# Optimization experiments

Hardware: AMD Instinct MI355X
Metric: run time of the kernel (lower is better)

Reference implementation:

```python
import jax, jax.numpy as jnp
import numpy as np

ALPHA = 0.15       # blend weight for merged mean vs center token
SIZE_DELTA = 0.0   # additive smoothing on cluster sizes


def setup_inputs() -> dict:
    key = jax.random.key(0)
    B, T, C = 8, 4096, 1024
    x = jax.random.normal(key, (B, T, C), dtype=jnp.float32)
    return {"x": x, "layer_idx": 0, "requested_r": 2048}


def reference(x, layer_idx, requested_r):
    B, T, C = x.shape
    K = max(1, T - int(requested_r))

    # token importance scores = squared L2 norm per token
    scores = jnp.sum(x * x, axis=-1)                      # [B, T]
    # CLS protection: force token 0 to be kept
    scores = scores.at[:, 0].set(jnp.finfo(scores.dtype).max)
    _, keep_idx = jax.lax.top_k(scores, K)                # [B, K]
    keep_idx = jnp.sort(keep_idx, axis=-1)

    # cosine nearest-kept-center assignment
    feat = x / (jnp.linalg.norm(x, axis=-1, keepdims=True) + 1e-12)  # [B, T, C]
    kept_feat = jnp.take_along_axis(feat, keep_idx[..., None], axis=1)  # [B, K, C]
    sim = jnp.einsum('bth,bkh->btk', feat, kept_feat)     # [B, T, K]
    assign_idx = jnp.argmax(sim, axis=-1)                 # [B, T]
    # force each kept center to self-assign (vectorized scatter,
    # replaces the original Python double for-loop with .item() syncs)
    b_idx = jnp.arange(B)[:, None]
    assign_idx = assign_idx.at[b_idx, keep_idx].set(jnp.arange(K)[None, :])

    # scatter-based size-weighted merge: segment mean over assigned tokens
    seg = (assign_idx + jnp.arange(B)[:, None] * K).reshape(-1)       # [B*T]
    sums = jax.ops.segment_sum(x.reshape(B * T, C), seg, num_segments=B * K)
    cnt = jax.ops.segment_sum(jnp.ones((B * T,), x.dtype), seg, num_segments=B * K)
    merged = (sums / (cnt[:, None] + SIZE_DELTA)).reshape(B, K, C)    # [B, K, C]

    x_kept = jnp.take_along_axis(x, keep_idx[..., None], axis=1)      # [B, K, C]
    out = (1.0 - ALPHA) * x_kept + ALPHA * merged
    return out
```

## Files before the change

kernel.cpp:

```cpp
#include <hip/hip_runtime.h>
#include <hip/hip_bf16.h>
#include <float.h>
#include <math.h>

constexpr int B_ = 8;
constexpr int T_ = 4096;
constexpr int C_ = 1024;
constexpr int K_ = 2048;
constexpr int MROWS = T_ - K_;

constexpr int BM = 128, BN = 128, BK = 64;
constexpr int NB = K_ / BN;
constexpr float REFINE_DELTA = 4e-4f;

typedef _Float16 f16x8 __attribute__((ext_vector_type(8)));
typedef float    f32x4 __attribute__((ext_vector_type(4)));

__device__ __forceinline__ void gload16(const ushort* g, ushort* l) {
  __builtin_amdgcn_global_load_lds(
      (const __attribute__((address_space(1))) unsigned int*)g,
      (__attribute__((address_space(3))) unsigned int*)l, 16, 0, 0);
}

__global__ __launch_bounds__(256) void split_score_kernel(
    const float* __restrict__ x, ushort* __restrict__ xh,
    double* __restrict__ sd, float* __restrict__ rnorm)
{
  int lane = threadIdx.x & 63, wave = threadIdx.x >> 6;
  int row = blockIdx.x * 4 + wave;
  size_t base = (size_t)row * C_;
  double s = 0.0;
  #pragma unroll
  for (int j = 0; j < 4; j++) {
    int i4 = j * 256 + lane * 4;
    float4 v = *reinterpret_cast<const float4*>(&x[base + i4]);
    ushort4 h;
    { _Float16 a = (_Float16)v.x; h.x = *(ushort*)&a; }
    { _Float16 a = (_Float16)v.y; h.y = *(ushort*)&a; }
    { _Float16 a = (_Float16)v.z; h.z = *(ushort*)&a; }
    { _Float16 a = (_Float16)v.w; h.w = *(ushort*)&a; }
    *reinterpret_cast<ushort4*>(&xh[base + i4]) = h;
    s += (double)v.x * v.x + (double)v.y * v.y
       + (double)v.z * v.z + (double)v.w * v.w;
  }
  #pragma unroll
  for (int off = 32; off > 0; off >>= 1) s += __shfl_down(s, off);
  if (lane == 0) {
    sd[row] = s;
    rnorm[row] = (float)(1.0 / (sqrt(s) + 1e-12));
  }
}

__global__ __launch_bounds__(256) void rank_kernel(
    const double* __restrict__ sd, int* __restrict__ flag)
{
  int b = blockIdx.y;
  __shared__ double sh[T_];
  for (int i = threadIdx.x; i < T_; i += 256)
    sh[i] = (i == 0) ? DBL_MAX : sd[b * T_ + i];
  __syncthreads();
  int t = blockIdx.x * 128 + (threadIdx.x >> 1);
  int half = threadIdx.x & 1;
  double key = sh[t];
  int cnt = 0;
  int j0 = half * 2048;
  #pragma unroll 4
  for (int jj = 0; jj < 2048; jj++) {
    int j = j0 + jj;
    double sj = sh[j];
    cnt += (sj > key) || (sj == key && j < t);
  }
  cnt += __shfl_xor(cnt, 1);
  if (half == 0) flag[b * T_ + t] = (cnt < K_) ? 1 : 0;
}

__global__ __launch_bounds__(256) void select_kernel(
    const int* __restrict__ flag, int* __restrict__ keep_idx,
    int* __restrict__ drop_idx, int* __restrict__ assign)
{
  int b = blockIdx.x, tid = threadIdx.x;
  __shared__ int sums[256];
  int f[16], s = 0;
  int base = b * T_ + tid * 16;
  #pragma unroll
  for (int i = 0; i < 16; i++) { f[i] = flag[base + i]; s += f[i]; }
  sums[tid] = s;
  __syncthreads();
  for (int off = 1; off < 256; off <<= 1) {
    int v = 0;
    if (tid >= off) v = sums[tid - off];
    __syncthreads();
    if (tid >= off) sums[tid] += v;
    __syncthreads();
  }
  int run = (tid == 0) ? 0 : sums[tid - 1];
  #pragma unroll
  for (int i = 0; i < 16; i++) {
    int t = tid * 16 + i;
    if (f[i]) { keep_idx[b * K_ + run] = t; assign[b * T_ + t] = run; run++; }
    else drop_idx[b * MROWS + (t - run)] = t;
  }
}

__global__ void zero_kernel(int* __restrict__ cnt, int* __restrict__ nref)
{
  int i = blockIdx.x * 256 + threadIdx.x;
  if (i < B_ * K_) cnt[i] = 0;
  if (i == 0) *nref = 0;
}

__global__ __launch_bounds__(256) void mfma_argmax_kernel(
    const ushort* __restrict__ xh, const float* __restrict__ rnorm,
    const int* __restrict__ keep_idx, const int* __restrict__ drop_idx,
    float* __restrict__ pb, float* __restrict__ ps, int* __restrict__ pk)
{
  __shared__ __align__(16) ushort lds[2][2][8][128][8];

  int b  = blockIdx.z;
  int m0 = blockIdx.y * BM;
  int n0 = blockIdx.x * BN;
  int tid = threadIdx.x;
  int lane = tid & 63, wave = tid >> 6;
  int quad = lane >> 4, col = lane & 15;
  int wm = wave >> 1, wn = wave & 1;

  int srow = tid & 127;
  int sc8  = (tid >> 7) * 8;

  int dtok_s = drop_idx[b * MROWS + m0 + srow];
  const ushort* ga = xh + (size_t)(b * T_ + dtok_s) * C_;
  int ktok_s = keep_idx[b * K_ + n0 + srow];
  const ushort* gb = xh + (size_t)(b * T_ + ktok_s) * C_;

  int ldst = tid * 8;

  float scale[4]; int ncand[4];
  #pragma unroll
  for (int j = 0; j < 4; j++) {
    int nn = n0 + wn * 64 + j * 16 + col;
    ncand[j] = nn;
    scale[j] = rnorm[b * T_ + keep_idx[b * K_ + nn]];
  }

  f32x4 acc[4][4];
  #pragma unroll
  for (int i = 0; i < 4; i++)
    #pragma unroll
    for (int j = 0; j < 4; j++) acc[i][j] = (f32x4)0.f;

  auto issue = [&](int k0, int st) {
    ushort* base = &lds[st][0][0][0][0];
    gload16(ga + k0 + sc8,      base + ldst);
    gload16(ga + k0 + 16 + sc8, base + ldst + 2048);
    gload16(ga + k0 + 32 + sc8, base + ldst + 4096);
    gload16(ga + k0 + 48 + sc8, base + ldst + 6144);
    ushort* bb = base + 8192;
    gload16(gb + k0 + sc8,      bb + ldst);
    gload16(gb + k0 + 16 + sc8, bb + ldst + 2048);
    gload16(gb + k0 + 32 + sc8, bb + ldst + 4096);
    gload16(gb + k0 + 48 + sc8, bb + ldst + 6144);
  };

  issue(0, 0);
  __syncthreads();

  for (int ks = 0; ks < C_ / BK; ks++) {
    int cur = ks & 1;
    if (ks < C_ / BK - 1) issue((ks + 1) * BK, cur ^ 1);

    #pragma unroll
    for (int s = 0; s < 2; s++) {
      f16x8 fa[4], fb[4];
      #pragma unroll
      for (int i = 0; i < 4; i++) {
        int row = wm * 64 + i * 16 + col;
        fa[i] = *reinterpret_cast<const f16x8*>(&lds[cur][0][s * 4 + quad][row][0]);
      }
      #pragma unroll
      for (int j = 0; j < 4; j++) {
        int row = wn * 64 + j * 16 + col;
        fb[j] = *reinterpret_cast<const f16x8*>(&lds[cur][1][s * 4 + quad][row][0]);
      }
      #pragma unroll
      for (int i = 0; i < 4; i++)
        #pragma unroll
        for (int j = 0; j < 4; j++)
          acc[i][j] = __builtin_amdgcn_mfma_f32_16x16x32_f16(fa[i], fb[j], acc[i][j], 0, 0, 0);
    }
    __syncthreads();
  }

  float* redb   = (float*)(&lds[0][0][0][0][0]);
  float* redsec = redb + 256;
  int*   redk   = (int*)(redb + 512);

  #pragma unroll
  for (int i = 0; i < 4; i++) {
    #pragma unroll
    for (int r = 0; r < 4; r++) {
      float b1 = -FLT_MAX, b2 = -FLT_MAX; int k1 = 0;
      #pragma unroll
      for (int j = 0; j < 4; j++) {
        float v = acc[i][j][r] * scale[j];
        if (v > b1) { b2 = b1; b1 = v; k1 = ncand[j]; }
        else if (v > b2) b2 = v;
      }
      #pragma unroll
      for (int off = 1; off < 16; off <<= 1) {
        float ob1 = __shfl_xor(b1, off);
        float ob2 = __shfl_xor(b2, off);
        int   ok1 = __shfl_xor(k1, off);
        if (ob1 > b1 || (ob1 == b1 && ok1 < k1)) { b2 = fmaxf(b1, ob2); b1 = ob1; k1 = ok1; }
        else b2 = fmaxf(b2, ob1);
      }
      if (col == 0) {
        int tl = wm * 64 + i * 16 + quad * 4 + r;
        redb[wn * 128 + tl] = b1; redsec[wn * 128 + tl] = b2; redk[wn * 128 + tl] = k1;
      }
    }
  }
  __syncthreads();
  if (tid < 128) {
    float b1 = redb[tid], b2 = redsec[tid]; int k1 = redk[tid];
    float o1 = redb[128 + tid], o2 = redsec[128 + tid]; int ok = redk[128 + tid];
    if (o1 > b1) { b2 = fmaxf(b1, o2); b1 = o1; k1 = ok; }
    else b2 = fmaxf(b2, o1);
    size_t p = ((size_t)(b * NB + blockIdx.x)) * MROWS + m0 + tid;
    pb[p] = b1; ps[p] = b2; pk[p] = k1;
  }
}

__global__ __launch_bounds__(256) void reduce2_kernel(
    const float* __restrict__ pb, const float* __restrict__ ps, const int* __restrict__ pk,
    const float* __restrict__ rnorm, const int* __restrict__ drop_idx,
    int* __restrict__ assign, int* __restrict__ rlist, int* __restrict__ nref)
{
  int idx2 = blockIdx.x * 256 + threadIdx.x;
  int b = idx2 >> 11;
  int rc = idx2 & (MROWS - 1);
  float b1 = -FLT_MAX, b2 = -FLT_MAX; int k1 = 0;
  for (int nb = 0; nb < NB; nb++) {
    size_t p = ((size_t)(b * NB + nb)) * MROWS + rc;
    float v = pb[p], s = ps[p]; int k = pk[p];
    if (v > b1) { b2 = fmaxf(b1, s); b1 = v; k1 = k; }
    else b2 = fmaxf(b2, v);
  }
  int t = drop_idx[idx2];
  assign[b * T_ + t] = k1;
  if ((b1 - b2) * rnorm[b * T_ + t] < REFINE_DELTA) {
    int qi = atomicAdd(nref, 1);
    rlist[qi] = idx2;
  }
}

__global__ __launch_bounds__(256) void refine_kernel(
    const float* __restrict__ x, const double* __restrict__ sd,
    const int* __restrict__ keep_idx, const int* __restrict__ drop_idx,
    const float* __restrict__ rnorm,
    const float* __restrict__ pb, const float* __restrict__ ps, const int* __restrict__ pk,
    const int* __restrict__ nref, const int* __restrict__ rlist, int* __restrict__ assign)
{
  __shared__ __align__(16) float xs[C_];
  __shared__ int cand[K_];
  __shared__ int ncand_s;
  __shared__ double wv[4];
  __shared__ int wk[4];
  __shared__ float spb[NB], sps[NB];
  __shared__ int spk[NB];
  int n = *nref;
  int lane = threadIdx.x & 63, wave = threadIdx.x >> 6;
  for (int qi = blockIdx.x; qi < n; qi += gridDim.x) {
    int idx2 = rlist[qi];
    int b = idx2 >> 11, rc = idx2 & (MROWS - 1);
    int t = drop_idx[idx2];
    int bt = b * T_ + t;
    __syncthreads();
    const float* xt = x + ((size_t)b * T_ + t) * C_;
    for (int i = threadIdx.x; i < C_; i += 256) xs[i] = xt[i];
    if (threadIdx.x < NB) {
      size_t p = ((size_t)(b * NB + threadIdx.x)) * MROWS + rc;
      spb[threadIdx.x] = pb[p]; sps[threadIdx.x] = ps[p]; spk[threadIdx.x] = pk[p];
    }
    __syncthreads();
    if (threadIdx.x == 0) {
      float b1 = -FLT_MAX;
      for (int nb = 0; nb < NB; nb++) if (spb[nb] > b1) b1 = spb[nb];
      float thr = b1 - REFINE_DELTA / rnorm[bt];
      int nc = 0;
      for (int nb = 0; nb < NB; nb++) {
        if (spb[nb] >= thr) {
          if (sps[nb] >= thr) { for (int j = 0; j < BN; j++) cand[nc++] = nb * BN + j; }
          else cand[nc++] = spk[nb];
        }
      }
      ncand_s = nc;
    }
    __syncthreads();
    int nc = ncand_s;
    double bv = -DBL_MAX; int bk = 0x7fffffff;
    for (int ci = wave; ci < nc; ci += 4) {
      int k = cand[ci];
      int kt = keep_idx[b * K_ + k];
      const float* xr = x + ((size_t)b * T_ + kt) * C_;
      double s = 0.0;
      int c0 = lane * 16;
      #pragma unroll
      for (int c = 0; c < 16; c += 4) {
        float4 v = *reinterpret_cast<const float4*>(&xr[c0 + c]);
        s += (double)xs[c0 + c]     * v.x + (double)xs[c0 + c + 1] * v.y
           + (double)xs[c0 + c + 2] * v.z + (double)xs[c0 + c + 3] * v.w;
      }
      #pragma unroll
      for (int off = 32; off > 0; off >>= 1) s += __shfl_down(s, off);
      s = __shfl(s, 0);
      s /= sqrt(sd[b * T_ + kt]);
      if (s > bv || (s == bv && k < bk)) { bv = s; bk = k; }
    }
    if (lane == 0) { wv[wave] = bv; wk[wave] = bk; }
    __syncthreads();
    if (threadIdx.x == 0) {
      double fb = wv[0]; int fk = wk[0];
      for (int w2 = 1; w2 < 4; w2++)
        if (wv[w2] > fb || (wv[w2] == fb && wk[w2] < fk)) { fb = wv[w2]; fk = wk[w2]; }
      assign[bt] = fk;
    }
  }
}

__global__ void count_kernel(const int* __restrict__ assign, int* __restrict__ cnt)
{
  int i = blockIdx.x * 256 + threadIdx.x;
  int b = i >> 12;
  atomicAdd(&cnt[b * K_ + assign[i]], 1);
}

__global__ __launch_bounds__(256) void scan_kernel(
    const int* __restrict__ cnt, int* __restrict__ offs, int* __restrict__ cursor)
{
  int b = blockIdx.x, tid = threadIdx.x;
  __shared__ int sums[256];
  int v[8], s = 0;
  int base = b * K_ + tid * 8;
  #pragma unroll
  for (int i = 0; i < 8; i++) { v[i] = cnt[base + i]; s += v[i]; }
  sums[tid] = s;
  __syncthreads();
  for (int off = 1; off < 256; off <<= 1) {
    int t2 = 0;
    if (tid >= off) t2 = sums[tid - off];
    __syncthreads();
    if (tid >= off) sums[tid] += t2;
    __syncthreads();
  }
  int run = (tid == 0) ? 0 : sums[tid - 1];
  #pragma unroll
  for (int i = 0; i < 8; i++) { offs[base + i] = run; cursor[base + i] = run; run += v[i]; }
}

__global__ void scatter_kernel(const int* __restrict__ assign,
                               int* __restrict__ cursor, int* __restrict__ lists)
{
  int i = blockIdx.x * 256 + threadIdx.x;
  int b = i >> 12, t = i & (T_ - 1);
  int p = atomicAdd(&cursor[b * K_ + assign[i]], 1);
  lists[b * T_ + p] = t;
}

__global__ __launch_bounds__(256) void merge_kernel(
    const float* __restrict__ x, const int* __restrict__ keep_idx,
    const int* __restrict__ cnt, const int* __restrict__ offs,
    const int* __restrict__ lists, float* __restrict__ out)
{
  __shared__ int toks[256];
  int b = blockIdx.y, k = blockIdx.x;
  int m = cnt[b * K_ + k], off = offs[b * K_ + k];
  const float* xb = x + (size_t)b * T_ * C_;
  int c4 = threadIdx.x * 4;
  float sx = 0.f, sy = 0.f, sz = 0.f, sw = 0.f;
  for (int basei = 0; basei < m; basei += 256) {
    int nchunk = min(256, m - basei);
    __syncthreads();
    if (threadIdx.x < nchunk) toks[threadIdx.x] = lists[b * T_ + off + basei + threadIdx.x];
    __syncthreads();
    for (int i = 0; i < nchunk; i++) {
      int tok = toks[i];
      float4 v = *reinterpret_cast<const float4*>(&xb[(size_t)tok * C_ + c4]);
      sx += v.x; sy += v.y; sz += v.z; sw += v.w;
    }
  }
  int kt = keep_idx[b * K_ + k];
  float4 xk = *reinterpret_cast<const float4*>(&xb[(size_t)kt * C_ + c4]);
  float fm = (float)m;
  float4 o;
  o.x = 0.85f * xk.x + 0.15f * (sx / fm);
  o.y = 0.85f * xk.y + 0.15f * (sy / fm);
  o.z = 0.85f * xk.z + 0.15f * (sz / fm);
  o.w = 0.85f * xk.w + 0.15f * (sw / fm);
  *reinterpret_cast<float4*>(&out[((size_t)b * K_ + k) * C_ + c4]) = o;
}

extern "C" void kernel_launch(void* const* d_in, const int* in_sizes, int n_in,
                              void* d_out, int out_size, void* d_ws, size_t ws_size,
                              hipStream_t stream)
{
  const float* x = (const float*)d_in[0];
  float* out = (float*)d_out;

  char* w = (char*)d_ws;
  ushort* xh    = (ushort*)w;  w += sizeof(ushort) * (size_t)B_ * T_ * C_;
  float* pb     = (float*)w;   w += sizeof(float) * (size_t)B_ * NB * MROWS;
  float* ps     = (float*)w;   w += sizeof(float) * (size_t)B_ * NB * MROWS;
  int*   pk     = (int*)w;     w += sizeof(int) * (size_t)B_ * NB * MROWS;
  double* sd    = (double*)w;  w += sizeof(double) * B_ * T_;
  float* rnorm  = (float*)w;   w += sizeof(float) * B_ * T_;
  int* flag     = (int*)w;     w += sizeof(int) * B_ * T_;
  int* keep_idx = (int*)w;     w += sizeof(int) * B_ * K_;
  int* drop_idx = (int*)w;     w += sizeof(int) * B_ * MROWS;
  int* assign   = (int*)w;     w += sizeof(int) * B_ * T_;
  int* cnt      = (int*)w;     w += sizeof(int) * B_ * K_;
  int* offs     = (int*)w;     w += sizeof(int) * B_ * K_;
  int* cursor   = (int*)w;     w += sizeof(int) * B_ * K_;
  int* lists    = (int*)w;     w += sizeof(int) * B_ * T_;
  int* rlist    = (int*)w;     w += sizeof(int) * B_ * MROWS;
  int* nref     = (int*)w;     w += 256;

  split_score_kernel<<<B_ * T_ / 4, 256, 0, stream>>>(x, xh, sd, rnorm);
  rank_kernel<<<dim3(T_ / 128, B_), 256, 0, stream>>>(sd, flag);
  select_kernel<<<B_, 256, 0, stream>>>(flag, keep_idx, drop_idx, assign);
  zero_kernel<<<(B_ * K_ + 255) / 256, 256, 0, stream>>>(cnt, nref);
  mfma_argmax_kernel<<<dim3(NB, MROWS / BM, B_), 256, 0, stream>>>(
      xh, rnorm, keep_idx, drop_idx, pb, ps, pk);
  reduce2_kernel<<<B_ * MROWS / 256, 256, 0, stream>>>(
      pb, ps, pk, rnorm, drop_idx, assign, rlist, nref);
  refine_kernel<<<256, 256, 0, stream>>>(
      x, sd, keep_idx, drop_idx, rnorm, pb, ps, pk, nref, rlist, assign);
  count_kernel<<<B_ * T_ / 256, 256, 0, stream>>>(assign, cnt);
  scan_kernel<<<B_, 256, 0, stream>>>(cnt, offs, cursor);
  scatter_kernel<<<B_ * T_ / 256, 256, 0, stream>>>(assign, cursor, lists);
  merge_kernel<<<dim3(K_, B_), 256, 0, stream>>>(x, keep_idx, cnt, offs, lists, out);
}
```

Before: 574.8 us.

## Triple-buffer MFMA argmax K-loop and fold cluster counting into reduce/refine

The GEMM-argmax main loop moves from a double-buffered BK=64 stage to a triple-buffered BK=32 pipeline. It uses explicit vmcnt waits and raw s_barrier so that two stages of global-to-LDS loads are in flight while MFMAs run. Separately, the count kernel is removed: counts start at 1 for kept centers, reduce2 atomically counts each dropped token's assignment, and refine adjusts counts when it changes an assignment. This saves a launch and a pass over assign, at the cost of more atomics and finer-grained barriers.

```diff
diff --git a/kernel.cpp b/kernel.cpp
--- a/kernel.cpp
+++ b/kernel.cpp
@@ -9,8 +9,9 @@
 constexpr int K_ = 2048;
 constexpr int MROWS = T_ - K_;
 
-constexpr int BM = 128, BN = 128, BK = 64;
+constexpr int BM = 128, BN = 128, BK = 32;
 constexpr int NB = K_ / BN;
+constexpr int NKS = C_ / BK;
 constexpr float REFINE_DELTA = 4e-4f;
 
 typedef _Float16 f16x8 __attribute__((ext_vector_type(8)));
@@ -105,7 +106,7 @@
 __global__ void zero_kernel(int* __restrict__ cnt, int* __restrict__ nref)
 {
   int i = blockIdx.x * 256 + threadIdx.x;
-  if (i < B_ * K_) cnt[i] = 0;
+  if (i < B_ * K_) cnt[i] = 1;
   if (i == 0) *nref = 0;
 }
 
@@ -114,7 +115,7 @@
     const int* __restrict__ keep_idx, const int* __restrict__ drop_idx,
     float* __restrict__ pb, float* __restrict__ ps, int* __restrict__ pk)
 {
-  __shared__ __align__(16) ushort lds[2][2][8][128][8];
+  __shared__ __align__(16) ushort lds[3][2][4][128][8];
 
   int b  = blockIdx.z;
   int m0 = blockIdx.y * BM;
@@ -148,46 +149,53 @@
     #pragma unroll
     for (int j = 0; j < 4; j++) acc[i][j] = (f32x4)0.f;
 
-  auto issue = [&](int k0, int st) {
-    ushort* base = &lds[st][0][0][0][0];
+  auto issue = [&](int stg) {
+    int k0 = stg * BK;
+    ushort* base = &lds[stg % 3][0][0][0][0];
     gload16(ga + k0 + sc8,      base + ldst);
     gload16(ga + k0 + 16 + sc8, base + ldst + 2048);
-    gload16(ga + k0 + 32 + sc8, base + ldst + 4096);
-    gload16(ga + k0 + 48 + sc8, base + ldst + 6144);
-    ushort* bb = base + 8192;
-    gload16(gb + k0 + sc8,      bb + ldst);
-    gload16(gb + k0 + 16 + sc8, bb + ldst + 2048);
-    gload16(gb + k0 + 32 + sc8, bb + ldst + 4096);
-    gload16(gb + k0 + 48 + sc8, bb + ldst + 6144);
+    gload16(gb + k0 + sc8,      base + 4096 + ldst);
+    gload16(gb + k0 + 16 + sc8, base + 4096 + ldst + 2048);
   };
 
-  issue(0, 0);
-  __syncthreads();
-
-  for (int ks = 0; ks < C_ / BK; ks++) {
-    int cur = ks & 1;
-    if (ks < C_ / BK - 1) issue((ks + 1) * BK, cur ^ 1);
-
+  issue(0);
+  issue(1);
+  asm volatile("s_waitcnt vmcnt(4)" ::: "memory");
+  __builtin_amdgcn_sched_barrier(0);
+  __builtin_amdgcn_s_barrier();
+  __builtin_amdgcn_sched_barrier(0);
+
+  for (int ks = 0; ks < NKS; ks++) {
+    int cur = ks % 3;
+    if (ks <= NKS - 3) issue(ks + 2);
+
+    f16x8 fa[4], fb[4];
     #pragma unroll
-    for (int s = 0; s < 2; s++) {
-      f16x8 fa[4], fb[4];
+    for (int i = 0; i < 4; i++) {
+      int row = wm * 64 + i * 16 + col;
+      fa[i] = *reinterpret_cast<const f16x8*>(&lds[cur][0][quad][row][0]);
+    }
+    #pragma unroll
+    for (int j = 0; j < 4; j++) {
+      int row = wn * 64 + j * 16 + col;
+      fb[j] = *reinterpret_cast<const f16x8*>(&lds[cur][1][quad][row][0]);
+    }
+    #pragma unroll
+    for (int i = 0; i < 4; i++)
       #pragma unroll
-      for (int i = 0; i < 4; i++) {
-        int row = wm * 64 + i * 16 + col;
-        fa[i] = *reinterpret_cast<const f16x8*>(&lds[cur][0][s * 4 + quad][row][0]);
-      }
-      #pragma unroll
-      for (int j = 0; j < 4; j++) {
-        int row = wn * 64 + j * 16 + col;
-        fb[j] = *reinterpret_cast<const f16x8*>(&lds[cur][1][s * 4 + quad][row][0]);
-      }
-      #pragma unroll
-      for (int i = 0; i < 4; i++)
-        #pragma unroll
-        for (int j = 0; j < 4; j++)
-          acc[i][j] = __builtin_amdgcn_mfma_f32_16x16x32_f16(fa[i], fb[j], acc[i][j], 0, 0, 0);
-    }
-    __syncthreads();
+      for (int j = 0; j < 4; j++)
+        acc[i][j] = __builtin_amdgcn_mfma_f32_16x16x32_f16(fa[i], fb[j], acc[i][j], 0, 0, 0);
+
+    if (ks <= NKS - 3) {
+      asm volatile("s_waitcnt vmcnt(4)" ::: "memory");
+    } else if (ks == NKS - 2) {
+      asm volatile("s_waitcnt vmcnt(0)" ::: "memory");
+    }
+    __builtin_amdgcn_sched_barrier(0);
+    if (ks < NKS - 1) {
+      __builtin_amdgcn_s_barrier();
+      __builtin_amdgcn_sched_barrier(0);
+    }
   }
 
   float* redb   = (float*)(&lds[0][0][0][0][0]);
@@ -233,7 +241,8 @@
 __global__ __launch_bounds__(256) void reduce2_kernel(
     const float* __restrict__ pb, const float* __restrict__ ps, const int* __restrict__ pk,
     const float* __restrict__ rnorm, const int* __restrict__ drop_idx,
-    int* __restrict__ assign, int* __restrict__ rlist, int* __restrict__ nref)
+    int* __restrict__ assign, int* __restrict__ cnt,
+    int* __restrict__ rlist, int* __restrict__ nref)
 {
   int idx2 = blockIdx.x * 256 + threadIdx.x;
   int b = idx2 >> 11;
@@ -247,6 +256,7 @@
   }
   int t = drop_idx[idx2];
   assign[b * T_ + t] = k1;
+  atomicAdd(&cnt[b * K_ + k1], 1);
   if ((b1 - b2) * rnorm[b * T_ + t] < REFINE_DELTA) {
     int qi = atomicAdd(nref, 1);
     rlist[qi] = idx2;
@@ -258,7 +268,8 @@
     const int* __restrict__ keep_idx, const int* __restrict__ drop_idx,
     const float* __restrict__ rnorm,
     const float* __restrict__ pb, const float* __restrict__ ps, const int* __restrict__ pk,
-    const int* __restrict__ nref, const int* __restrict__ rlist, int* __restrict__ assign)
+    const int* __restrict__ nref, const int* __restrict__ rlist,
+    int* __restrict__ assign, int* __restrict__ cnt)
 {
   __shared__ __align__(16) float xs[C_];
   __shared__ int cand[K_];
@@ -322,16 +333,14 @@
       double fb = wv[0]; int fk = wk[0];
       for (int w2 = 1; w2 < 4; w2++)
         if (wv[w2] > fb || (wv[w2] == fb && wk[w2] < fk)) { fb = wv[w2]; fk = wk[w2]; }
-      assign[bt] = fk;
-    }
-  }
-}
-
-__global__ void count_kernel(const int* __restrict__ assign, int* __restrict__ cnt)
-{
-  int i = blockIdx.x * 256 + threadIdx.x;
-  int b = i >> 12;
-  atomicAdd(&cnt[b * K_ + assign[i]], 1);
+      int old = assign[bt];
+      if (fk != old) {
+        atomicSub(&cnt[b * K_ + old], 1);
+        atomicAdd(&cnt[b * K_ + fk], 1);
+        assign[bt] = fk;
+      }
+    }
+  }
 }
 
 __global__ __launch_bounds__(256) void scan_kernel(
@@ -431,10 +440,9 @@
   mfma_argmax_kernel<<<dim3(NB, MROWS / BM, B_), 256, 0, stream>>>(
       xh, rnorm, keep_idx, drop_idx, pb, ps, pk);
   reduce2_kernel<<<B_ * MROWS / 256, 256, 0, stream>>>(
-      pb, ps, pk, rnorm, drop_idx, assign, rlist, nref);
+      pb, ps, pk, rnorm, drop_idx, assign, cnt, rlist, nref);
   refine_kernel<<<256, 256, 0, stream>>>(
-      x, sd, keep_idx, drop_idx, rnorm, pb, ps, pk, nref, rlist, assign);
-  count_kernel<<<B_ * T_ / 256, 256, 0, stream>>>(assign, cnt);
+      x, sd, keep_idx, drop_idx, rnorm, pb, ps, pk, nref, rlist, assign, cnt);
   scan_kernel<<<B_, 256, 0, stream>>>(cnt, offs, cursor);
   scatter_kernel<<<B_ * T_ / 256, 256, 0, stream>>>(assign, cursor, lists);
   merge_kernel<<<dim3(K_, B_), 256, 0, stream>>>(x, keep_idx, cnt, offs, lists, out);
```

Result: faster. 558.0 us (-2.9%).
